# Kernel tuning notes

Hardware: AMD Instinct MI355X
Metric: run time of the kernel (lower is better)

Reference implementation:

```python
import jax, jax.numpy as jnp
import numpy as np

B, VMAX, EGO, H, ACT = 2048, 128, 15, 256, 2


def _u(k, shape, fan):
    s = 1.0 / np.sqrt(fan)
    return jax.random.uniform(k, shape, jnp.float32, -s, s)


def setup_inputs() -> dict:
    key = jax.random.key(0)
    ks = jax.random.split(key, 20)
    return {
        "state": jax.random.normal(ks[0], (B, VMAX, EGO), jnp.float32),
        "lengths": jax.random.randint(ks[1], (B,), 1, VMAX + 1),
        "Wih1": _u(ks[2], (4 * H, EGO), H), "Whh1": _u(ks[3], (4 * H, H), H),
        "bih1": _u(ks[4], (4 * H,), H), "bhh1": _u(ks[5], (4 * H,), H),
        "W1": _u(ks[6], (1024, H), H), "b1": _u(ks[7], (1024,), H),
        "W2": _u(ks[8], (1024, 1024), 1024), "b2": _u(ks[9], (1024,), 1024),
        "W3": _u(ks[10], (512, 1024), 1024), "b3": _u(ks[11], (512,), 1024),
        "W4": _u(ks[12], (256, 512), 512), "b4": _u(ks[13], (256,), 512),
        "Wih2": _u(ks[14], (4 * H, H), H), "Whh2": _u(ks[15], (4 * H, H), H),
        "bih2": _u(ks[16], (4 * H,), H), "bhh2": _u(ks[17], (4 * H,), H),
        "Wpi": _u(ks[18], (ACT, H), H), "bpi": _u(ks[19], (ACT,), H),
    }


def lstm_cell(x, h, c, Wih, Whh, bih, bhh):
    # torch.nn.LSTMCell: gates ordered i, f, g, o
    g = x @ Wih.T + bih + h @ Whh.T + bhh  # [B, 4H]
    i, f, gg, o = jnp.split(g, 4, axis=-1)
    c = jax.nn.sigmoid(f) * c + jax.nn.sigmoid(i) * jnp.tanh(gg)
    h = jax.nn.sigmoid(o) * jnp.tanh(c)
    return h, c


def reference(state, lengths, Wih1, Whh1, bih1, bhh1, W1, b1, W2, b2,
              W3, b3, W4, b4, Wih2, Whh2, bih2, bhh2, Wpi, bpi):
    Bn, V, _ = state.shape
    z = jnp.zeros((Bn, H), state.dtype)

    # Encoder: per-vehicle LSTM over ragged lengths (masked updates).
    def enc_step(carry, xs):
        h, c = carry
        x_t, t = xs
        hn, cn = lstm_cell(x_t, h, c, Wih1, Whh1, bih1, bhh1)
        m = (t < lengths)[:, None]
        return (jnp.where(m, hn, h), jnp.where(m, cn, c)), None
    (h, _), _ = jax.lax.scan(enc_step, (z, z),
                             (state.transpose(1, 0, 2), jnp.arange(V)))

    x = jax.nn.relu(h @ W1.T + b1)
    x = jax.nn.relu(x @ W2.T + b2)
    x = jax.nn.relu(x @ W3.T + b3)
    x = jax.nn.relu(x @ W4.T + b4)  # [B, 256]

    # Decoder: repeats the SAME input x each step; action = tanh(pi(cx))
    # (original applies pi to the cell state cx, kept faithful).
    def dec_step(carry, _):
        h, c = carry
        hn, cn = lstm_cell(x, h, c, Wih2, Whh2, bih2, bhh2)
        act = jnp.tanh(cn @ Wpi.T + bpi)
        return (hn, cn), act
    _, acts = jax.lax.scan(dec_step, (z, z), None, length=V)  # [V, B, ACT]
    acts = acts.transpose(1, 0, 2)  # [B, V, ACT]

    # Zero out padded timesteps (ragged output represented as padded dense).
    mask = (jnp.arange(V)[None, :] < lengths[:, None])[..., None]
    return acts * mask.astype(acts.dtype)
```

## Files before the change

### kernel.cpp

```cpp
#include <hip/hip_runtime.h>

typedef _Float16 f16;
typedef _Float16 f16x8 __attribute__((ext_vector_type(8)));
typedef float f32x4 __attribute__((ext_vector_type(4)));

#define MFMA(a,b,c) __builtin_amdgcn_mfma_f32_16x16x32_f16(a,b,c,0,0,0)

constexpr int B_ = 2048, V_ = 128, EGO_ = 15, H_ = 256;
constexpr int MT = 16;
constexpr int ENC_KT = 9;
constexpr int DEC_KT = 8;
constexpr int ENC_KR = 5;
constexpr int DEC_KR = 4;
constexpr int HSTR = 296;
constexpr int DSTR = 264;


__device__ __forceinline__ float sigf(float x){ return 1.f/(1.f+__expf(-x)); }
__device__ __forceinline__ float tanh_fast(float x){ return 1.f - 2.f/(1.f+__expf(2.f*x)); }

__device__ __forceinline__ void st_u32(uint32_t* p, uint32_t v){
    __hip_atomic_store(p, v, __ATOMIC_RELAXED, __HIP_MEMORY_SCOPE_AGENT);
}
__device__ __forceinline__ uint32_t ld_u32(const uint32_t* p){
    return __hip_atomic_load(p, __ATOMIC_RELAXED, __HIP_MEMORY_SCOPE_AGENT);
}
union cvt8 { f16x8 h; uint32_t u[4]; };

__global__ void prepack_enc(const float* __restrict__ Whh1, const float* __restrict__ Wih1,
                            f16* __restrict__ dst){
    int id = blockIdx.x*256 + threadIdx.x;
    if (id >= 2*4*8*ENC_KT*64) return;
    int L = id & 63; int c = id >> 6;
    int kt = c % ENC_KT; c /= ENC_KT;
    int nt = c & 7; c >>= 3;
    int w = c & 3; int hb = c >> 2;
    int n = (nt>>1)*256 + hb*128 + w*32 + (nt&1)*16 + (L&15);
    int kbase = kt*32 + (L>>4)*8;
    #pragma unroll
    for (int j=0;j<8;++j){
        int k = kbase + j;
        float x = (k < 256) ? Whh1[n*256 + k] : ((k < 271) ? Wih1[n*15 + (k-256)] : 0.f);
        dst[(size_t)id*8 + j] = (f16)x;
    }
}
__global__ void prepack_dec(const float* __restrict__ Whh2, f16* __restrict__ dst){
    int id = blockIdx.x*256 + threadIdx.x;
    if (id >= 2*4*8*DEC_KT*64) return;
    int L = id & 63; int c = id >> 6;
    int kt = c % DEC_KT; c /= DEC_KT;
    int nt = c & 7; c >>= 3;
    int w = c & 3; int hb = c >> 2;
    int n = (nt>>1)*256 + hb*128 + w*32 + (nt&1)*16 + (L&15);
    int kbase = kt*32 + (L>>4)*8;
    #pragma unroll
    for (int j=0;j<8;++j) dst[(size_t)id*8 + j] = (f16)Whh2[n*256 + kbase + j];
}
__global__ void bias_kernel(const float* bih1,const float* bhh1,const float* bih2,
                            const float* bhh2,float* be,float* bd){
    int i = blockIdx.x*256 + threadIdx.x;
    if (i < 1024){ be[i]=bih1[i]+bhh1[i]; bd[i]=bih2[i]+bhh2[i]; }
}
__global__ void convert_kernel(const float* __restrict__ src, f16* __restrict__ dst, int n){
    int i = blockIdx.x*256 + threadIdx.x;
    if (i < n) dst[i] = (f16)src[i];
}

__global__ __launch_bounds__(256,1) void encoder_kernel(
    const float* __restrict__ state, const int* __restrict__ lengths,
    const f16* __restrict__ Wp, const float* __restrict__ bias,
    f16* __restrict__ henc, f16* __restrict__ ebuf, int* __restrict__ flags)
{
    __shared__ __align__(16) f16 wlds[4*8*(ENC_KT-ENC_KR)*64*8];
    __shared__ __align__(16) f16 hcat[MT*HSTR];
    const int tid = threadIdx.x;
    const int wave = tid>>6, lane = tid&63, lr = lane&15, quad = lane>>4;
    const int bid = blockIdx.x, hb = bid>>7, g = bid&127, pbid = bid^128;
    const int row0 = g*MT;
    const int xr = tid>>4, xc = tid&15;

    for (int i=tid;i<MT*HSTR;i+=256) hcat[i] = (f16)0.f;

    int len_r[4];
    #pragma unroll
    for (int r=0;r<4;++r) len_r[r] = lengths[row0 + quad*4 + r];

    float bias_v[8];
    #pragma unroll
    for (int nt=0;nt<8;++nt)
        bias_v[nt] = bias[(nt>>1)*256 + hb*128 + wave*32 + (nt&1)*16 + lr];

    const f16x8* Wb = (const f16x8*)Wp + (size_t)((hb*4+wave)*8*ENC_KT)*64;
    f16x8 wreg[8][ENC_KR];
    #pragma unroll
    for (int nt=0;nt<8;++nt)
        #pragma unroll
        for (int kt=0;kt<ENC_KR;++kt)
            wreg[nt][kt] = Wb[(nt*ENC_KT + kt)*64 + lane];
    f16x8* wl = (f16x8*)wlds + (size_t)wave*(8*(ENC_KT-ENC_KR)*64);
    #pragma unroll
    for (int nt=0;nt<8;++nt)
        #pragma unroll
        for (int kt=0;kt<ENC_KT-ENC_KR;++kt)
            wl[(nt*(ENC_KT-ENC_KR) + kt)*64 + lane] = Wb[(nt*ENC_KT + ENC_KR + kt)*64 + lane];

    float c_reg[8], h_reg[8];
    #pragma unroll
    for (int i=0;i<8;++i){ c_reg[i]=0.f; h_reg[i]=0.f; }

    for (int t=0;t<V_;++t){
        if (tid < 240){
            int rr = tid/15, cc = tid - rr*15;
            hcat[rr*HSTR + 256 + cc] = (f16)state[(size_t)(row0+rr)*V_*EGO_ + t*EGO_ + cc];
        }
        __syncthreads();
        f32x4 acc[8];
        #pragma unroll
        for (int nt=0;nt<8;++nt) acc[nt] = (f32x4){bias_v[nt],bias_v[nt],bias_v[nt],bias_v[nt]};
        #pragma unroll
        for (int kt=0;kt<ENC_KR;++kt){
            f16x8 a = *(const f16x8*)&hcat[lr*HSTR + kt*32 + quad*8];
            #pragma unroll
            for (int nt=0;nt<8;++nt) acc[nt] = MFMA(a, wreg[nt][kt], acc[nt]);
        }
        #pragma unroll
        for (int kt=0;kt<ENC_KT-ENC_KR;++kt){
            f16x8 a = *(const f16x8*)&hcat[lr*HSTR + (ENC_KR+kt)*32 + quad*8];
            #pragma unroll
            for (int nt=0;nt<8;++nt)
                acc[nt] = MFMA(a, wl[(nt*(ENC_KT-ENC_KR) + kt)*64 + lane], acc[nt]);
        }
        __syncthreads();
        #pragma unroll
        for (int s=0;s<2;++s){
            #pragma unroll
            for (int r=0;r<4;++r){
                int idx = s*4 + r;
                float gi = acc[s][r],   gf = acc[2+s][r];
                float gg = acc[4+s][r], go = acc[6+s][r];
                float cn = sigf(gf)*c_reg[idx] + sigf(gi)*tanh_fast(gg);
                float hn = sigf(go)*tanh_fast(cn);
                bool upd = (t < len_r[r]);
                c_reg[idx] = upd ? cn : c_reg[idx];
                h_reg[idx] = upd ? hn : h_reg[idx];
                hcat[(quad*4+r)*HSTR + hb*128 + wave*32 + s*16 + lr] = (f16)h_reg[idx];
            }
        }
        __syncthreads();
        {
            cvt8 cv; cv.h = *(const f16x8*)&hcat[xr*HSTR + hb*128 + xc*8];
            uint32_t* dst = (uint32_t*)(ebuf + ((size_t)(t&1)*256 + bid)*2048) + xr*64 + xc*4;
            st_u32(dst+0,cv.u[0]); st_u32(dst+1,cv.u[1]);
            st_u32(dst+2,cv.u[2]); st_u32(dst+3,cv.u[3]);
        }
        __syncthreads();
        if (tid == 0){
            st_u32((uint32_t*)&flags[bid], (uint32_t)(t+1));
            while (ld_u32((const uint32_t*)&flags[pbid]) < (uint32_t)(t+1))
                __builtin_amdgcn_s_sleep(2);
        }
        __syncthreads();
        {
            const uint32_t* src = (const uint32_t*)(ebuf + ((size_t)(t&1)*256 + pbid)*2048) + xr*64 + xc*4;
            cvt8 cv;
            cv.u[0]=ld_u32(src+0); cv.u[1]=ld_u32(src+1);
            cv.u[2]=ld_u32(src+2); cv.u[3]=ld_u32(src+3);
            *(f16x8*)&hcat[xr*HSTR + (1-hb)*128 + xc*8] = cv.h;
        }
    }
    #pragma unroll
    for (int s=0;s<2;++s)
        #pragma unroll
        for (int r=0;r<4;++r)
            henc[(size_t)(row0+quad*4+r)*H_ + hb*128 + wave*32 + s*16 + lr] = (f16)h_reg[s*4+r];
}

template<bool RELU, bool F32OUT>
__global__ __launch_bounds__(256,2) void gemm_kernel(
    const f16* __restrict__ A, const f16* __restrict__ W,
    const float* __restrict__ bias, void* __restrict__ outp,
    int M, int N, int K)
{
    constexpr int ASTR = 40;
    __shared__ __align__(16) f16 As[64*ASTR];
    __shared__ __align__(16) f16 Ws[64*ASTR];
    const int tid = threadIdx.x;
    const int wave = tid>>6, lane = tid&63, lr = lane&15, quad = lane>>4;
    const int n0 = blockIdx.x*64, m0 = blockIdx.y*64;
    const int lrow = tid>>2, lk8 = (tid&3)*8;

    f32x4 acc[4];
    #pragma unroll
    for (int mt=0;mt<4;++mt) acc[mt] = (f32x4){0.f,0.f,0.f,0.f};

    for (int k0=0;k0<K;k0+=32){
        __syncthreads();
        *(f16x8*)&As[lrow*ASTR + lk8] = *(const f16x8*)&A[(size_t)(m0+lrow)*K + k0 + lk8];
        *(f16x8*)&Ws[lrow*ASTR + lk8] = *(const f16x8*)&W[(size_t)(n0+lrow)*K + k0 + lk8];
        __syncthreads();
        f16x8 b = *(const f16x8*)&Ws[(wave*16+lr)*ASTR + quad*8];
        #pragma unroll
        for (int mt=0;mt<4;++mt){
            f16x8 a = *(const f16x8*)&As[(mt*16+lr)*ASTR + quad*8];
            acc[mt] = MFMA(a, b, acc[mt]);
        }
    }
    float bv = bias[n0 + wave*16 + lr];
    #pragma unroll
    for (int mt=0;mt<4;++mt){
        #pragma unroll
        for (int r=0;r<4;++r){
            float v = acc[mt][r] + bv;
            if (RELU) v = fmaxf(v, 0.f);
            int m = m0 + mt*16 + quad*4 + r, n = n0 + wave*16 + lr;
            if (F32OUT) ((float*)outp)[(size_t)m*N + n] = v;
            else        ((f16*)outp)[(size_t)m*N + n] = (f16)v;
        }
    }
}

__global__ __launch_bounds__(256,1) void decoder_kernel(
    const int* __restrict__ lengths, const f16* __restrict__ Wp,
    const float* __restrict__ xdec, const float* __restrict__ Wpi,
    const float* __restrict__ bpi, float* __restrict__ out,
    f16* __restrict__ ebuf, int* __restrict__ flags, float* __restrict__ pbuf)
{
    __shared__ __align__(16) f16 wlds[4*8*(DEC_KT-DEC_KR)*64*8];
    __shared__ __align__(16) f16 hbuf[MT*DSTR];
    __shared__ float part[4][16][2];
    const int tid = threadIdx.x;
    const int wave = tid>>6, lane = tid&63, lr = lane&15, quad = lane>>4;
    const int bid = blockIdx.x, hb = bid>>7, g = bid&127, pbid = bid^128;
    const int row0 = g*MT;
    const int xr = tid>>4, xc = tid&15;

    for (int i=tid;i<MT*DSTR;i+=256) hbuf[i] = (f16)0.f;

    float xd[8][4];
    #pragma unroll
    for (int nt=0;nt<8;++nt){
        int n = (nt>>1)*256 + hb*128 + wave*32 + (nt&1)*16 + lr;
        #pragma unroll
        for (int r=0;r<4;++r) xd[nt][r] = xdec[(size_t)(row0+quad*4+r)*1024 + n];
    }
    float wpi_reg[2][2];
    #pragma unroll
    for (int a=0;a<2;++a)
        #pragma unroll
        for (int s=0;s<2;++s)
            wpi_reg[a][s] = Wpi[a*H_ + hb*128 + wave*32 + s*16 + lr];

    const f16x8* Wb = (const f16x8*)Wp + (size_t)((hb*4+wave)*8*DEC_KT)*64;
    f16x8 wreg[8][DEC_KR];
    #pragma unroll
    for (int nt=0;nt<8;++nt)
        #pragma unroll
        for (int kt=0;kt<DEC_KR;++kt)
            wreg[nt][kt] = Wb[(nt*DEC_KT + kt)*64 + lane];
    f16x8* wl = (f16x8*)wlds + (size_t)wave*(8*(DEC_KT-DEC_KR)*64);
    #pragma unroll
    for (int nt=0;nt<8;++nt)
        #pragma unroll
        for (int kt=0;kt<DEC_KT-DEC_KR;++kt)
            wl[(nt*(DEC_KT-DEC_KR) + kt)*64 + lane] = Wb[(nt*DEC_KT + DEC_KR + kt)*64 + lane];

    float c_reg[8];
    #pragma unroll
    for (int i=0;i<8;++i) c_reg[i]=0.f;

    const int m_o = (tid>>1)&15, a_o = tid&1;
    const float bpi_o = bpi[a_o];
    const int len_o = (tid<32) ? lengths[row0+m_o] : 0;
    const size_t outbase = (size_t)(row0+m_o)*V_*2 + a_o;

    for (int t=0;t<V_;++t){
        __syncthreads();
        f32x4 acc[8];
        #pragma unroll
        for (int nt=0;nt<8;++nt) acc[nt] = (f32x4){xd[nt][0],xd[nt][1],xd[nt][2],xd[nt][3]};
        #pragma unroll
        for (int kt=0;kt<DEC_KR;++kt){
            f16x8 a = *(const f16x8*)&hbuf[lr*DSTR + kt*32 + quad*8];
            #pragma unroll
            for (int nt=0;nt<8;++nt) acc[nt] = MFMA(a, wreg[nt][kt], acc[nt]);
        }
        #pragma unroll
        for (int kt=0;kt<DEC_KT-DEC_KR;++kt){
            f16x8 a = *(const f16x8*)&hbuf[lr*DSTR + (DEC_KR+kt)*32 + quad*8];
            #pragma unroll
            for (int nt=0;nt<8;++nt)
                acc[nt] = MFMA(a, wl[(nt*(DEC_KT-DEC_KR) + kt)*64 + lane], acc[nt]);
        }
        __syncthreads();
        float spi[4][2];
        #pragma unroll
        for (int r=0;r<4;++r){ spi[r][0]=0.f; spi[r][1]=0.f; }
        #pragma unroll
        for (int s=0;s<2;++s){
            #pragma unroll
            for (int r=0;r<4;++r){
                int idx = s*4 + r;
                float gi = acc[s][r],   gf = acc[2+s][r];
                float gg = acc[4+s][r], go = acc[6+s][r];
                float cn = sigf(gf)*c_reg[idx] + sigf(gi)*tanh_fast(gg);
                c_reg[idx] = cn;
                float hn = sigf(go)*tanh_fast(cn);
                hbuf[(quad*4+r)*DSTR + hb*128 + wave*32 + s*16 + lr] = (f16)hn;
                spi[r][0] += cn*wpi_reg[0][s];
                spi[r][1] += cn*wpi_reg[1][s];
            }
        }
        #pragma unroll
        for (int msk=1; msk<16; msk<<=1){
            #pragma unroll
            for (int r=0;r<4;++r){
                spi[r][0] += __shfl_xor(spi[r][0], msk, 64);
                spi[r][1] += __shfl_xor(spi[r][1], msk, 64);
            }
        }
        if (lr == 0){
            #pragma unroll
            for (int r=0;r<4;++r){
                part[wave][quad*4+r][0] = spi[r][0];
                part[wave][quad*4+r][1] = spi[r][1];
            }
        }
        __syncthreads();
        {
            cvt8 cv; cv.h = *(const f16x8*)&hbuf[xr*DSTR + hb*128 + xc*8];
            uint32_t* dst = (uint32_t*)(ebuf + ((size_t)(t&1)*256 + bid)*2048) + xr*64 + xc*4;
            st_u32(dst+0,cv.u[0]); st_u32(dst+1,cv.u[1]);
            st_u32(dst+2,cv.u[2]); st_u32(dst+3,cv.u[3]);
        }
        if (hb == 1 && tid < 32){
            float v = part[0][m_o][a_o]+part[1][m_o][a_o]+part[2][m_o][a_o]+part[3][m_o][a_o];
            st_u32((uint32_t*)pbuf + ((size_t)(t&1)*128 + g)*32 + tid, __float_as_uint(v));
        }
        __syncthreads();
        if (tid == 0){
            st_u32((uint32_t*)&flags[bid], (uint32_t)(t+1));
            while (ld_u32((const uint32_t*)&flags[pbid]) < (uint32_t)(t+1))
                __builtin_amdgcn_s_sleep(2);
        }
        __syncthreads();
        {
            const uint32_t* src = (const uint32_t*)(ebuf + ((size_t)(t&1)*256 + pbid)*2048) + xr*64 + xc*4;
            cvt8 cv;
            cv.u[0]=ld_u32(src+0); cv.u[1]=ld_u32(src+1);
            cv.u[2]=ld_u32(src+2); cv.u[3]=ld_u32(src+3);
            *(f16x8*)&hbuf[xr*DSTR + (1-hb)*128 + xc*8] = cv.h;
        }
        if (hb == 0 && tid < 32){
            uint32_t pu = ld_u32((const uint32_t*)pbuf + ((size_t)(t&1)*128 + g)*32 + tid);
            float v = part[0][m_o][a_o] + part[1][m_o][a_o]
                    + part[2][m_o][a_o] + part[3][m_o][a_o]
                    + __uint_as_float(pu) + bpi_o;
            v = tanh_fast(v);
            out[outbase + (size_t)t*2] = (t < len_o) ? v : 0.f;
        }
    }
}

extern "C" void kernel_launch(void* const* d_in, const int* in_sizes, int n_in,
                              void* d_out, int out_size, void* d_ws, size_t ws_size,
                              hipStream_t stream) {
    const float* state = (const float*)d_in[0];
    const int*   lengths=(const int*)d_in[1];
    const float* Wih1 = (const float*)d_in[2];
    const float* Whh1 = (const float*)d_in[3];
    const float* bih1 = (const float*)d_in[4];
    const float* bhh1 = (const float*)d_in[5];
    const float* W1   = (const float*)d_in[6];  const float* b1 = (const float*)d_in[7];
    const float* W2   = (const float*)d_in[8];  const float* b2 = (const float*)d_in[9];
    const float* W3   = (const float*)d_in[10]; const float* b3 = (const float*)d_in[11];
    const float* W4   = (const float*)d_in[12]; const float* b4 = (const float*)d_in[13];
    const float* Wih2 = (const float*)d_in[14]; const float* Whh2=(const float*)d_in[15];
    const float* bih2 = (const float*)d_in[16]; const float* bhh2=(const float*)d_in[17];
    const float* Wpi  = (const float*)d_in[18]; const float* bpi =(const float*)d_in[19];
    float* out = (float*)d_out;

    char* p = (char*)d_ws;
    auto alloc = [&](size_t bytes){ char* r = p; p += (bytes + 255) & ~(size_t)255; return r; };
    f16* WencP   = (f16*)alloc((size_t)2*4*8*ENC_KT*64*8*2);
    f16* WdecP   = (f16*)alloc((size_t)2*4*8*DEC_KT*64*8*2);
    f16* W1f     = (f16*)alloc((size_t)1024*256*2);
    f16* W2f     = (f16*)alloc((size_t)1024*1024*2);
    f16* W3f     = (f16*)alloc((size_t)512*1024*2);
    f16* W4f     = (f16*)alloc((size_t)256*512*2);
    f16* Wih2f   = (f16*)alloc((size_t)1024*256*2);
    float* biasE = (float*)alloc(1024*4);
    float* biasD = (float*)alloc(1024*4);
    f16* henc    = (f16*)alloc((size_t)2048*256*2);
    f16* act1    = (f16*)alloc((size_t)2048*1024*2);
    f16* act2    = (f16*)alloc((size_t)2048*1024*2);
    f16* act3    = (f16*)alloc((size_t)2048*512*2);
    f16* x4      = (f16*)alloc((size_t)2048*256*2);
    float* xdec  = (float*)alloc((size_t)2048*1024*4);
    f16* ebuf    = (f16*)alloc((size_t)2*256*2048*2);
    float* pbuf  = (float*)alloc((size_t)2*128*32*4);
    int* flags   = (int*)alloc((size_t)512*4);

    hipMemsetAsync(flags, 0, 512*4, stream);

    prepack_enc<<<(2*4*8*ENC_KT*64+255)/256,256,0,stream>>>(Whh1, Wih1, WencP);
    prepack_dec<<<(2*4*8*DEC_KT*64+255)/256,256,0,stream>>>(Whh2, WdecP);
    bias_kernel<<<4,256,0,stream>>>(bih1,bhh1,bih2,bhh2,biasE,biasD);
    convert_kernel<<<(1024*256+255)/256,256,0,stream>>>(W1, W1f, 1024*256);
    convert_kernel<<<(1024*1024+255)/256,256,0,stream>>>(W2, W2f, 1024*1024);
    convert_kernel<<<(512*1024+255)/256,256,0,stream>>>(W3, W3f, 512*1024);
    convert_kernel<<<(256*512+255)/256,256,0,stream>>>(W4, W4f, 256*512);
    convert_kernel<<<(1024*256+255)/256,256,0,stream>>>(Wih2, Wih2f, 1024*256);

    encoder_kernel<<<256,256,0,stream>>>(state, lengths, WencP, biasE, henc, ebuf, flags);

    gemm_kernel<true ,false><<<dim3(16,32),256,0,stream>>>(henc, W1f, b1, act1, 2048,1024,256);
    gemm_kernel<true ,false><<<dim3(16,32),256,0,stream>>>(act1, W2f, b2, act2, 2048,1024,1024);
    gemm_kernel<true ,false><<<dim3( 8,32),256,0,stream>>>(act2, W3f, b3, act3, 2048, 512,1024);
    gemm_kernel<true ,false><<<dim3( 4,32),256,0,stream>>>(act3, W4f, b4, x4,   2048, 256, 512);
    gemm_kernel<false,true ><<<dim3(16,32),256,0,stream>>>(x4, Wih2f, biasD, xdec, 2048,1024,256);

    decoder_kernel<<<256,256,0,stream>>>(lengths, WdecP, xdec, Wpi, bpi, out,
                                         ebuf, flags+256, pbuf);
}
```

Baseline: 1.359 ms.

## Restructure LSTM partner exchange with per-wave flags, direct global loads, and Lmax truncation

Reorders the K dimension of the packed recurrent weights so each block handles its own hidden half first. The partner block's half is read straight from global memory with cache-bypassing loads into MFMA operands rather than staged through LDS, which lets the own-half MFMAs overlap the wait for the partner. The single-thread flag spin and extra barriers are replaced by per-wave flags that each wave polls itself. Both loops stop at the group's maximum length, padded outputs are zero-filled, and the decoder output write is deferred one step so the partner's partial sum is not waited on. This removes several barriers and LDS round trips per step, but relies on inline asm cache-control bits for coherence.

```diff
diff --git a/kernel.cpp b/kernel.cpp
--- a/kernel.cpp
+++ b/kernel.cpp
@@ -10,10 +10,8 @@
 constexpr int MT = 16;
 constexpr int ENC_KT = 9;
 constexpr int DEC_KT = 8;
-constexpr int ENC_KR = 5;
-constexpr int DEC_KR = 4;
-constexpr int HSTR = 296;
-constexpr int DSTR = 264;
+constexpr int HSTR = 168;
+constexpr int DSTR = 136;
 
 
 __device__ __forceinline__ float sigf(float x){ return 1.f/(1.f+__expf(-x)); }
@@ -25,7 +23,25 @@
 __device__ __forceinline__ uint32_t ld_u32(const uint32_t* p){
     return __hip_atomic_load(p, __ATOMIC_RELAXED, __HIP_MEMORY_SCOPE_AGENT);
 }
-union cvt8 { f16x8 h; uint32_t u[4]; };
+__device__ __forceinline__ void bypass_ld4(f16x8& d0, f16x8& d1, f16x8& d2, f16x8& d3,
+                                           const f16* p0, const f16* p1,
+                                           const f16* p2, const f16* p3){
+    asm volatile(
+        "global_load_dwordx4 %0, %4, off sc0 sc1\n\t"
+        "global_load_dwordx4 %1, %5, off sc0 sc1\n\t"
+        "global_load_dwordx4 %2, %6, off sc0 sc1\n\t"
+        "global_load_dwordx4 %3, %7, off sc0 sc1\n\t"
+        "s_waitcnt vmcnt(0)"
+        : "=&v"(d0), "=&v"(d1), "=&v"(d2), "=&v"(d3)
+        : "v"(p0), "v"(p1), "v"(p2), "v"(p3)
+        : "memory");
+}
+__device__ __forceinline__ void bypass_st(f16* p, f16x8 v){
+    asm volatile("global_store_dwordx4 %0, %1, off sc0 sc1" :: "v"(p), "v"(v) : "memory");
+}
+__device__ __forceinline__ void vm_drain(){
+    asm volatile("s_waitcnt vmcnt(0)" ::: "memory");
+}
 
 __global__ void prepack_enc(const float* __restrict__ Whh1, const float* __restrict__ Wih1,
                             f16* __restrict__ dst){
@@ -36,10 +52,14 @@
     int nt = c & 7; c >>= 3;
     int w = c & 3; int hb = c >> 2;
     int n = (nt>>1)*256 + hb*128 + w*32 + (nt&1)*16 + (L&15);
-    int kbase = kt*32 + (L>>4)*8;
+    int kb = (L>>4)*8;
     #pragma unroll
     for (int j=0;j<8;++j){
-        int k = kbase + j;
+        int kin = kb + j;
+        int k;
+        if (kt < 4)      k = hb*128 + kt*32 + kin;
+        else if (kt < 8) k = (1-hb)*128 + (kt-4)*32 + kin;
+        else             k = 256 + kin;
         float x = (k < 256) ? Whh1[n*256 + k] : ((k < 271) ? Wih1[n*15 + (k-256)] : 0.f);
         dst[(size_t)id*8 + j] = (f16)x;
     }
@@ -52,9 +72,13 @@
     int nt = c & 7; c >>= 3;
     int w = c & 3; int hb = c >> 2;
     int n = (nt>>1)*256 + hb*128 + w*32 + (nt&1)*16 + (L&15);
-    int kbase = kt*32 + (L>>4)*8;
-    #pragma unroll
-    for (int j=0;j<8;++j) dst[(size_t)id*8 + j] = (f16)Whh2[n*256 + kbase + j];
+    int kb = (L>>4)*8;
+    #pragma unroll
+    for (int j=0;j<8;++j){
+        int kin = kb + j;
+        int k = (kt < 4) ? (hb*128 + kt*32 + kin) : ((1-hb)*128 + (kt-4)*32 + kin);
+        dst[(size_t)id*8 + j] = (f16)Whh2[n*256 + k];
+    }
 }
 __global__ void bias_kernel(const float* bih1,const float* bhh1,const float* bih2,
                             const float* bhh2,float* be,float* bd){
@@ -71,8 +95,9 @@
     const f16* __restrict__ Wp, const float* __restrict__ bias,
     f16* __restrict__ henc, f16* __restrict__ ebuf, int* __restrict__ flags)
 {
-    __shared__ __align__(16) f16 wlds[4*8*(ENC_KT-ENC_KR)*64*8];
+    __shared__ __align__(16) f16 wlds[4*8*4*64*8];
     __shared__ __align__(16) f16 hcat[MT*HSTR];
+    __shared__ int lmax_s;
     const int tid = threadIdx.x;
     const int wave = tid>>6, lane = tid&63, lr = lane&15, quad = lane>>4;
     const int bid = blockIdx.x, hb = bid>>7, g = bid&127, pbid = bid^128;
@@ -80,6 +105,12 @@
     const int xr = tid>>4, xc = tid&15;
 
     for (int i=tid;i<MT*HSTR;i+=256) hcat[i] = (f16)0.f;
+    if (tid < 64){
+        int l = (lane<16) ? lengths[row0+lane] : 0;
+        #pragma unroll
+        for (int m=1;m<16;m<<=1){ int o = __shfl_xor(l, m, 64); l = (o>l)?o:l; }
+        if (lane==0) lmax_s = l;
+    }
 
     int len_r[4];
     #pragma unroll
@@ -91,44 +122,72 @@
         bias_v[nt] = bias[(nt>>1)*256 + hb*128 + wave*32 + (nt&1)*16 + lr];
 
     const f16x8* Wb = (const f16x8*)Wp + (size_t)((hb*4+wave)*8*ENC_KT)*64;
-    f16x8 wreg[8][ENC_KR];
+    f16x8 wreg[8][5];
+    #pragma unroll
+    for (int nt=0;nt<8;++nt){
+        #pragma unroll
+        for (int kt=0;kt<4;++kt) wreg[nt][kt] = Wb[(nt*ENC_KT + kt)*64 + lane];
+        wreg[nt][4] = Wb[(nt*ENC_KT + 8)*64 + lane];
+    }
+    f16x8* wl = (f16x8*)wlds + (size_t)wave*(8*4*64);
     #pragma unroll
     for (int nt=0;nt<8;++nt)
         #pragma unroll
-        for (int kt=0;kt<ENC_KR;++kt)
-            wreg[nt][kt] = Wb[(nt*ENC_KT + kt)*64 + lane];
-    f16x8* wl = (f16x8*)wlds + (size_t)wave*(8*(ENC_KT-ENC_KR)*64);
-    #pragma unroll
-    for (int nt=0;nt<8;++nt)
-        #pragma unroll
-        for (int kt=0;kt<ENC_KT-ENC_KR;++kt)
-            wl[(nt*(ENC_KT-ENC_KR) + kt)*64 + lane] = Wb[(nt*ENC_KT + ENC_KR + kt)*64 + lane];
-
+        for (int p=0;p<4;++p)
+            wl[(nt*4 + p)*64 + lane] = Wb[(nt*ENC_KT + 4 + p)*64 + lane];
+
+    __syncthreads();
+    const int rr = tid/15, cc = tid - rr*15;
+    const size_t xbase = (size_t)(row0+rr)*V_*EGO_ + cc;
+    float xreg = 0.f;
+    if (tid < 240){
+        hcat[rr*HSTR + 128 + cc] = (f16)state[xbase];
+        xreg = state[xbase + EGO_];
+    }
     float c_reg[8], h_reg[8];
     #pragma unroll
     for (int i=0;i<8;++i){ c_reg[i]=0.f; h_reg[i]=0.f; }
-
-    for (int t=0;t<V_;++t){
-        if (tid < 240){
-            int rr = tid/15, cc = tid - rr*15;
-            hcat[rr*HSTR + 256 + cc] = (f16)state[(size_t)(row0+rr)*V_*EGO_ + t*EGO_ + cc];
-        }
-        __syncthreads();
+    __syncthreads();
+    const int Lmax = lmax_s;
+
+    for (int t=0;t<Lmax;++t){
+        uint32_t f0 = (uint32_t)t;
+        if (t > 0 && lane < 4) f0 = ld_u32((const uint32_t*)&flags[pbid*4 + lane]);
         f32x4 acc[8];
         #pragma unroll
         for (int nt=0;nt<8;++nt) acc[nt] = (f32x4){bias_v[nt],bias_v[nt],bias_v[nt],bias_v[nt]};
         #pragma unroll
-        for (int kt=0;kt<ENC_KR;++kt){
+        for (int kt=0;kt<4;++kt){
             f16x8 a = *(const f16x8*)&hcat[lr*HSTR + kt*32 + quad*8];
             #pragma unroll
             for (int nt=0;nt<8;++nt) acc[nt] = MFMA(a, wreg[nt][kt], acc[nt]);
         }
-        #pragma unroll
-        for (int kt=0;kt<ENC_KT-ENC_KR;++kt){
-            f16x8 a = *(const f16x8*)&hcat[lr*HSTR + (ENC_KR+kt)*32 + quad*8];
-            #pragma unroll
-            for (int nt=0;nt<8;++nt)
-                acc[nt] = MFMA(a, wl[(nt*(ENC_KT-ENC_KR) + kt)*64 + lane], acc[nt]);
+        {
+            f16x8 a = *(const f16x8*)&hcat[lr*HSTR + 128 + quad*8];
+            #pragma unroll
+            for (int nt=0;nt<8;++nt) acc[nt] = MFMA(a, wreg[nt][4], acc[nt]);
+        }
+        if (t > 0){
+            f16x8 b0[8];
+            #pragma unroll
+            for (int nt=0;nt<8;++nt) b0[nt] = wl[(nt*4 + 0)*64 + lane];
+            if (lane < 4){
+                while (f0 < (uint32_t)t){
+                    __builtin_amdgcn_s_sleep(1);
+                    f0 = ld_u32((const uint32_t*)&flags[pbid*4 + lane]);
+                }
+            }
+            const f16* src = ebuf + ((size_t)((t-1)&1)*256 + pbid)*2048 + lr*128 + quad*8;
+            f16x8 a0,a1,a2,a3;
+            bypass_ld4(a0,a1,a2,a3, src, src+32, src+64, src+96);
+            #pragma unroll
+            for (int nt=0;nt<8;++nt) acc[nt] = MFMA(a0, b0[nt], acc[nt]);
+            #pragma unroll
+            for (int nt=0;nt<8;++nt) acc[nt] = MFMA(a1, wl[(nt*4+1)*64+lane], acc[nt]);
+            #pragma unroll
+            for (int nt=0;nt<8;++nt) acc[nt] = MFMA(a2, wl[(nt*4+2)*64+lane], acc[nt]);
+            #pragma unroll
+            for (int nt=0;nt<8;++nt) acc[nt] = MFMA(a3, wl[(nt*4+3)*64+lane], acc[nt]);
         }
         __syncthreads();
         #pragma unroll
@@ -143,29 +202,21 @@
                 bool upd = (t < len_r[r]);
                 c_reg[idx] = upd ? cn : c_reg[idx];
                 h_reg[idx] = upd ? hn : h_reg[idx];
-                hcat[(quad*4+r)*HSTR + hb*128 + wave*32 + s*16 + lr] = (f16)h_reg[idx];
-            }
-        }
+                hcat[(quad*4+r)*HSTR + wave*32 + s*16 + lr] = (f16)h_reg[idx];
+            }
+        }
+        if (tid < 240) hcat[rr*HSTR + 128 + cc] = (f16)xreg;
         __syncthreads();
         {
-            cvt8 cv; cv.h = *(const f16x8*)&hcat[xr*HSTR + hb*128 + xc*8];
-            uint32_t* dst = (uint32_t*)(ebuf + ((size_t)(t&1)*256 + bid)*2048) + xr*64 + xc*4;
-            st_u32(dst+0,cv.u[0]); st_u32(dst+1,cv.u[1]);
-            st_u32(dst+2,cv.u[2]); st_u32(dst+3,cv.u[3]);
-        }
-        __syncthreads();
-        if (tid == 0){
-            st_u32((uint32_t*)&flags[bid], (uint32_t)(t+1));
-            while (ld_u32((const uint32_t*)&flags[pbid]) < (uint32_t)(t+1))
-                __builtin_amdgcn_s_sleep(2);
-        }
-        __syncthreads();
-        {
-            const uint32_t* src = (const uint32_t*)(ebuf + ((size_t)(t&1)*256 + pbid)*2048) + xr*64 + xc*4;
-            cvt8 cv;
-            cv.u[0]=ld_u32(src+0); cv.u[1]=ld_u32(src+1);
-            cv.u[2]=ld_u32(src+2); cv.u[3]=ld_u32(src+3);
-            *(f16x8*)&hcat[xr*HSTR + (1-hb)*128 + xc*8] = cv.h;
+            f16x8 h8 = *(const f16x8*)&hcat[xr*HSTR + xc*8];
+            f16* dst = ebuf + ((size_t)(t&1)*256 + bid)*2048 + xr*128 + xc*8;
+            bypass_st(dst, h8);
+        }
+        vm_drain();
+        if (lane == 0) st_u32((uint32_t*)&flags[bid*4 + wave], (uint32_t)(t+1));
+        if (tid < 240){
+            int tn = (t+2 < V_) ? (t+2) : (V_-1);
+            xreg = state[xbase + (size_t)tn*EGO_];
         }
     }
     #pragma unroll
@@ -225,9 +276,10 @@
     const float* __restrict__ bpi, float* __restrict__ out,
     f16* __restrict__ ebuf, int* __restrict__ flags, float* __restrict__ pbuf)
 {
-    __shared__ __align__(16) f16 wlds[4*8*(DEC_KT-DEC_KR)*64*8];
+    __shared__ __align__(16) f16 wlds[4*8*4*64*8];
     __shared__ __align__(16) f16 hbuf[MT*DSTR];
     __shared__ float part[4][16][2];
+    __shared__ int lmax_s;
     const int tid = threadIdx.x;
     const int wave = tid>>6, lane = tid&63, lr = lane&15, quad = lane>>4;
     const int bid = blockIdx.x, hb = bid>>7, g = bid&127, pbid = bid^128;
@@ -235,6 +287,12 @@
     const int xr = tid>>4, xc = tid&15;
 
     for (int i=tid;i<MT*DSTR;i+=256) hbuf[i] = (f16)0.f;
+    if (tid < 64){
+        int l = (lane<16) ? lengths[row0+lane] : 0;
+        #pragma unroll
+        for (int m=1;m<16;m<<=1){ int o = __shfl_xor(l, m, 64); l = (o>l)?o:l; }
+        if (lane==0) lmax_s = l;
+    }
 
     float xd[8][4];
     #pragma unroll
@@ -251,18 +309,18 @@
             wpi_reg[a][s] = Wpi[a*H_ + hb*128 + wave*32 + s*16 + lr];
 
     const f16x8* Wb = (const f16x8*)Wp + (size_t)((hb*4+wave)*8*DEC_KT)*64;
-    f16x8 wreg[8][DEC_KR];
+    f16x8 wreg[8][4];
     #pragma unroll
     for (int nt=0;nt<8;++nt)
         #pragma unroll
-        for (int kt=0;kt<DEC_KR;++kt)
+        for (int kt=0;kt<4;++kt)
             wreg[nt][kt] = Wb[(nt*DEC_KT + kt)*64 + lane];
-    f16x8* wl = (f16x8*)wlds + (size_t)wave*(8*(DEC_KT-DEC_KR)*64);
+    f16x8* wl = (f16x8*)wlds + (size_t)wave*(8*4*64);
     #pragma unroll
     for (int nt=0;nt<8;++nt)
         #pragma unroll
-        for (int kt=0;kt<DEC_KT-DEC_KR;++kt)
-            wl[(nt*(DEC_KT-DEC_KR) + kt)*64 + lane] = Wb[(nt*DEC_KT + DEC_KR + kt)*64 + lane];
+        for (int p=0;p<4;++p)
+            wl[(nt*4 + p)*64 + lane] = Wb[(nt*DEC_KT + 4 + p)*64 + lane];
 
     float c_reg[8];
     #pragma unroll
@@ -272,24 +330,50 @@
     const float bpi_o = bpi[a_o];
     const int len_o = (tid<32) ? lengths[row0+m_o] : 0;
     const size_t outbase = (size_t)(row0+m_o)*V_*2 + a_o;
-
-    for (int t=0;t<V_;++t){
-        __syncthreads();
+    float own_prev = 0.f;
+
+    __syncthreads();
+    const int Lmax = lmax_s;
+
+    for (int t=0;t<Lmax;++t){
+        uint32_t f0 = (uint32_t)t;
+        if (t > 0 && lane < 4) f0 = ld_u32((const uint32_t*)&flags[pbid*4 + lane]);
         f32x4 acc[8];
         #pragma unroll
         for (int nt=0;nt<8;++nt) acc[nt] = (f32x4){xd[nt][0],xd[nt][1],xd[nt][2],xd[nt][3]};
         #pragma unroll
-        for (int kt=0;kt<DEC_KR;++kt){
+        for (int kt=0;kt<4;++kt){
             f16x8 a = *(const f16x8*)&hbuf[lr*DSTR + kt*32 + quad*8];
             #pragma unroll
             for (int nt=0;nt<8;++nt) acc[nt] = MFMA(a, wreg[nt][kt], acc[nt]);
         }
-        #pragma unroll
-        for (int kt=0;kt<DEC_KT-DEC_KR;++kt){
-            f16x8 a = *(const f16x8*)&hbuf[lr*DSTR + (DEC_KR+kt)*32 + quad*8];
-            #pragma unroll
-            for (int nt=0;nt<8;++nt)
-                acc[nt] = MFMA(a, wl[(nt*(DEC_KT-DEC_KR) + kt)*64 + lane], acc[nt]);
+        if (t > 0){
+            f16x8 b0[8];
+            #pragma unroll
+            for (int nt=0;nt<8;++nt) b0[nt] = wl[(nt*4 + 0)*64 + lane];
+            if (lane < 4){
+                while (f0 < (uint32_t)t){
+                    __builtin_amdgcn_s_sleep(1);
+                    f0 = ld_u32((const uint32_t*)&flags[pbid*4 + lane]);
+                }
+            }
+            const f16* src = ebuf + ((size_t)((t-1)&1)*256 + pbid)*2048 + lr*128 + quad*8;
+            f16x8 a0,a1,a2,a3;
+            bypass_ld4(a0,a1,a2,a3, src, src+32, src+64, src+96);
+            #pragma unroll
+            for (int nt=0;nt<8;++nt) acc[nt] = MFMA(a0, b0[nt], acc[nt]);
+            #pragma unroll
+            for (int nt=0;nt<8;++nt) acc[nt] = MFMA(a1, wl[(nt*4+1)*64+lane], acc[nt]);
+            #pragma unroll
+            for (int nt=0;nt<8;++nt) acc[nt] = MFMA(a2, wl[(nt*4+2)*64+lane], acc[nt]);
+            #pragma unroll
+            for (int nt=0;nt<8;++nt) acc[nt] = MFMA(a3, wl[(nt*4+3)*64+lane], acc[nt]);
+            if (hb == 0 && tid < 32){
+                uint32_t pu = ld_u32((const uint32_t*)pbuf + ((size_t)((t-1)&1)*128 + g)*32 + tid);
+                float v = own_prev + __uint_as_float(pu) + bpi_o;
+                v = tanh_fast(v);
+                out[outbase + (size_t)(t-1)*2] = ((t-1) < len_o) ? v : 0.f;
+            }
         }
         __syncthreads();
         float spi[4][2];
@@ -305,7 +389,7 @@
                 float cn = sigf(gf)*c_reg[idx] + sigf(gi)*tanh_fast(gg);
                 c_reg[idx] = cn;
                 float hn = sigf(go)*tanh_fast(cn);
-                hbuf[(quad*4+r)*DSTR + hb*128 + wave*32 + s*16 + lr] = (f16)hn;
+                hbuf[(quad*4+r)*DSTR + wave*32 + s*16 + lr] = (f16)hn;
                 spi[r][0] += cn*wpi_reg[0][s];
                 spi[r][1] += cn*wpi_reg[1][s];
             }
@@ -327,37 +411,30 @@
         }
         __syncthreads();
         {
-            cvt8 cv; cv.h = *(const f16x8*)&hbuf[xr*DSTR + hb*128 + xc*8];
-            uint32_t* dst = (uint32_t*)(ebuf + ((size_t)(t&1)*256 + bid)*2048) + xr*64 + xc*4;
-            st_u32(dst+0,cv.u[0]); st_u32(dst+1,cv.u[1]);
-            st_u32(dst+2,cv.u[2]); st_u32(dst+3,cv.u[3]);
-        }
-        if (hb == 1 && tid < 32){
-            float v = part[0][m_o][a_o]+part[1][m_o][a_o]+part[2][m_o][a_o]+part[3][m_o][a_o];
-            st_u32((uint32_t*)pbuf + ((size_t)(t&1)*128 + g)*32 + tid, __float_as_uint(v));
-        }
-        __syncthreads();
-        if (tid == 0){
-            st_u32((uint32_t*)&flags[bid], (uint32_t)(t+1));
-            while (ld_u32((const uint32_t*)&flags[pbid]) < (uint32_t)(t+1))
-                __builtin_amdgcn_s_sleep(2);
-        }
-        __syncthreads();
-        {
-            const uint32_t* src = (const uint32_t*)(ebuf + ((size_t)(t&1)*256 + pbid)*2048) + xr*64 + xc*4;
-            cvt8 cv;
-            cv.u[0]=ld_u32(src+0); cv.u[1]=ld_u32(src+1);
-            cv.u[2]=ld_u32(src+2); cv.u[3]=ld_u32(src+3);
-            *(f16x8*)&hbuf[xr*DSTR + (1-hb)*128 + xc*8] = cv.h;
-        }
-        if (hb == 0 && tid < 32){
-            uint32_t pu = ld_u32((const uint32_t*)pbuf + ((size_t)(t&1)*128 + g)*32 + tid);
-            float v = part[0][m_o][a_o] + part[1][m_o][a_o]
-                    + part[2][m_o][a_o] + part[3][m_o][a_o]
-                    + __uint_as_float(pu) + bpi_o;
-            v = tanh_fast(v);
-            out[outbase + (size_t)t*2] = (t < len_o) ? v : 0.f;
-        }
+            f16x8 h8 = *(const f16x8*)&hbuf[xr*DSTR + xc*8];
+            f16* dst = ebuf + ((size_t)(t&1)*256 + bid)*2048 + xr*128 + xc*8;
+            bypass_st(dst, h8);
+        }
+        if (tid < 32){
+            float own4 = part[0][m_o][a_o]+part[1][m_o][a_o]+part[2][m_o][a_o]+part[3][m_o][a_o];
+            if (hb == 1) st_u32((uint32_t*)pbuf + ((size_t)(t&1)*128 + g)*32 + tid,
+                                __float_as_uint(own4));
+            else         own_prev = own4;
+        }
+        vm_drain();
+        if (lane == 0) st_u32((uint32_t*)&flags[bid*4 + wave], (uint32_t)(t+1));
+    }
+    if (hb == 0 && tid < 32){
+        uint32_t fv = ld_u32((const uint32_t*)&flags[pbid*4 + 0]);
+        while (fv < (uint32_t)Lmax){
+            __builtin_amdgcn_s_sleep(1);
+            fv = ld_u32((const uint32_t*)&flags[pbid*4 + 0]);
+        }
+        uint32_t pu = ld_u32((const uint32_t*)pbuf + ((size_t)((Lmax-1)&1)*128 + g)*32 + tid);
+        float v = own_prev + __uint_as_float(pu) + bpi_o;
+        v = tanh_fast(v);
+        out[outbase + (size_t)(Lmax-1)*2] = ((Lmax-1) < len_o) ? v : 0.f;
+        for (int t=Lmax; t<V_; ++t) out[outbase + (size_t)t*2] = 0.f;
     }
 }
 
@@ -398,9 +475,9 @@
     float* xdec  = (float*)alloc((size_t)2048*1024*4);
     f16* ebuf    = (f16*)alloc((size_t)2*256*2048*2);
     float* pbuf  = (float*)alloc((size_t)2*128*32*4);
-    int* flags   = (int*)alloc((size_t)512*4);
-
-    hipMemsetAsync(flags, 0, 512*4, stream);
+    int* flags   = (int*)alloc((size_t)2048*4);
+
+    hipMemsetAsync(flags, 0, 2048*4, stream);
 
     prepack_enc<<<(2*4*8*ENC_KT*64+255)/256,256,0,stream>>>(Whh1, Wih1, WencP);
     prepack_dec<<<(2*4*8*DEC_KT*64+255)/256,256,0,stream>>>(Whh2, WdecP);
@@ -420,5 +497,5 @@
     gemm_kernel<false,true ><<<dim3(16,32),256,0,stream>>>(x4, Wih2f, biasD, xdec, 2048,1024,256);
 
     decoder_kernel<<<256,256,0,stream>>>(lengths, WdecP, xdec, Wpi, bpi, out,
-                                         ebuf, flags+256, pbuf);
-}
+                                         ebuf, flags+1024, pbuf);
+}
```

Result: faster. 1.316 ms (-3.2%).
